# Kernel optimization log

Hardware: AMD Instinct MI355X
Metric: run time of the kernel (lower is better)

Reference implementation:

```python
import jax, jax.numpy as jnp
import numpy as np


def _fake_quant(x, clip_val, level):
    """PACT-style non-negative fake quantization with STE on rounding.

    clamp to [0, clip_val], quantize to `level` uniform levels, dequantize.
    """
    c = clip_val.reshape(())
    scale = c / (level - 1)
    xc = jnp.clip(x, 0.0, c)
    q = jnp.round(xc / scale) * scale
    # straight-through: forward value is q, gradient flows through xc
    return xc + jax.lax.stop_gradient(q - xc)


def setup_inputs() -> dict:
    key = jax.random.key(0)
    k1, k2 = jax.random.split(key)
    B, M, K, N = 8, 4096, 64, 4096
    x1 = jax.random.uniform(k1, (B, M, K), dtype=jnp.float32)
    x2 = jax.random.uniform(k2, (B, K, N), dtype=jnp.float32)
    clip_val1 = jnp.ones((1,), dtype=jnp.float32)
    clip_val2 = jnp.ones((1,), dtype=jnp.float32)
    return {"x1": x1, "x2": x2, "clip_val1": clip_val1,
            "clip_val2": clip_val2, "level": 256}


def reference(x1, x2, clip_val1, clip_val2, level):
    q1 = _fake_quant(x1, clip_val1, level)  # [B, M, K]
    q2 = _fake_quant(x2, clip_val2, level)  # [B, K, N]
    return jnp.matmul(q1, q2)               # [B, M, N]
```

## Files before the change

### kernel.cpp

```cpp
#include <hip/hip_runtime.h>
#include <hip/hip_bf16.h>


#define BATCH 8
#define MDIM 4096
#define KDIM 64
#define NDIM 4096

typedef __attribute__((ext_vector_type(4))) unsigned short u16x4;
typedef __attribute__((ext_vector_type(8))) short s16x8;
typedef __attribute__((ext_vector_type(4))) float f32x4;

__device__ __forceinline__ unsigned short qcode(float x, float c, float inv) {
    float xc = fminf(fmaxf(x, 0.0f), c);
    float k = rintf(xc * inv);
    return (unsigned short)(__float_as_uint(k) >> 16);
}

#define QA_BLOCKS 2048

__global__ void quant_both(const float* __restrict__ x1, const float* __restrict__ x2,
                           unsigned short* __restrict__ qA, unsigned short* __restrict__ qBt,
                           const float* __restrict__ c1p, const float* __restrict__ c2p,
                           const int* __restrict__ lvp) {
    __shared__ unsigned short T[64 * 68];
    const int t = threadIdx.x;
    const float lvm1 = (float)(lvp[0] - 1);

    if (blockIdx.x < QA_BLOCKS) {
        const float c = c1p[0], inv = lvm1 / c;
        int i = blockIdx.x * 256 + t;
        float4 v = ((const float4*)x1)[i];
        u16x4 o;
        o[0] = qcode(v.x, c, inv);
        o[1] = qcode(v.y, c, inv);
        o[2] = qcode(v.z, c, inv);
        o[3] = qcode(v.w, c, inv);
        ((u16x4*)qA)[i] = o;
        return;
    }

    const float c = c2p[0], inv = lvm1 / c;
    int bi = blockIdx.x - QA_BLOCKS;
    int b = bi >> 6;
    int n0 = (bi & 63) * 64;

    const float* src = x2 + (size_t)b * KDIM * NDIM + n0;
#pragma unroll
    for (int it = 0; it < 4; ++it) {
        int qi = t + it * 256;
        int k = qi >> 4, c4 = qi & 15;
        float4 v = *(const float4*)(src + (size_t)k * NDIM + c4 * 4);
        u16x4 o;
        o[0] = qcode(v.x, c, inv);
        o[1] = qcode(v.y, c, inv);
        o[2] = qcode(v.z, c, inv);
        o[3] = qcode(v.w, c, inv);
        *(u16x4*)&T[k * 68 + c4 * 4] = o;
    }
    __syncthreads();

    unsigned short* dst = qBt + ((size_t)b * NDIM + n0) * KDIM;
#pragma unroll
    for (int it = 0; it < 4; ++it) {
        int qi = t + it * 256;
        int n = qi >> 4, c4 = qi & 15;
        u16x4 o;
        o[0] = T[(c4 * 4 + 0) * 68 + n];
        o[1] = T[(c4 * 4 + 1) * 68 + n];
        o[2] = T[(c4 * 4 + 2) * 68 + n];
        o[3] = T[(c4 * 4 + 3) * 68 + n];
        *(u16x4*)(dst + (size_t)n * KDIM + c4 * 4) = o;
    }
}

__global__ __launch_bounds__(256)
void gemm_q(const unsigned short* __restrict__ qA, const unsigned short* __restrict__ qBt,
            const float* __restrict__ c1p, const float* __restrict__ c2p,
            const int* __restrict__ lvp, float* __restrict__ out) {
    const int b = blockIdx.z, mt = blockIdx.y, nt = blockIdx.x;
    const int t = threadIdx.x;
    const int lane = t & 63, w = t >> 6;
    const int wr = (w >> 1) * 64, wc = (w & 1) * 64;
    const int r16 = lane & 15, kq = lane >> 4;

    const unsigned short* pA =
        qA + ((size_t)b * MDIM + mt * 128 + wr + r16) * KDIM + kq * 8;
    const unsigned short* pB =
        qBt + ((size_t)b * NDIM + nt * 128 + wc + r16) * KDIM + kq * 8;

    f32x4 acc[4][4] = {};
#pragma unroll
    for (int ks = 0; ks < 2; ++ks) {
        s16x8 a[4], bf[4];
#pragma unroll
        for (int mf = 0; mf < 4; ++mf)
            a[mf] = *(const s16x8*)(pA + mf * 16 * KDIM + ks * 32);
#pragma unroll
        for (int nf = 0; nf < 4; ++nf)
            bf[nf] = *(const s16x8*)(pB + nf * 16 * KDIM + ks * 32);
#pragma unroll
        for (int mf = 0; mf < 4; ++mf)
#pragma unroll
            for (int nf = 0; nf < 4; ++nf)
                acc[mf][nf] = __builtin_amdgcn_mfma_f32_16x16x32_bf16(
                    bf[nf], a[mf], acc[mf][nf], 0, 0, 0);
    }

    const float c1 = c1p[0], c2 = c2p[0];
    const float lvm1 = (float)(lvp[0] - 1);
    const float s = (c1 / lvm1) * (c2 / lvm1);

    size_t obase = (size_t)b * MDIM * NDIM;
    const int m0 = mt * 128 + wr, n0 = nt * 128 + wc;
#pragma unroll
    for (int mf = 0; mf < 4; ++mf) {
        int m = m0 + mf * 16 + r16;
        float* orow = out + obase + (size_t)m * NDIM;
#pragma unroll
        for (int nf = 0; nf < 4; ++nf) {
            int nb = n0 + nf * 16 + kq * 4;
            float4 v;
            v.x = acc[mf][nf][0] * s;
            v.y = acc[mf][nf][1] * s;
            v.z = acc[mf][nf][2] * s;
            v.w = acc[mf][nf][3] * s;
            *(float4*)(orow + nb) = v;
        }
    }
}

extern "C" void kernel_launch(void* const* d_in, const int* in_sizes, int n_in,
                              void* d_out, int out_size, void* d_ws, size_t ws_size,
                              hipStream_t stream) {
    const float* x1 = (const float*)d_in[0];
    const float* x2 = (const float*)d_in[1];
    const float* c1 = (const float*)d_in[2];
    const float* c2 = (const float*)d_in[3];
    const int* lv   = (const int*)d_in[4];
    float* out = (float*)d_out;

    unsigned short* qA = (unsigned short*)d_ws;
    unsigned short* qB = qA + (size_t)BATCH * MDIM * KDIM;

    quant_both<<<QA_BLOCKS + BATCH * (NDIM / 64), 256, 0, stream>>>(
        x1, x2, qA, qB, c1, c2, lv);
    gemm_q<<<dim3(NDIM / 128, MDIM / 128, BATCH), 256, 0, stream>>>(
        qA, qB, c1, c2, lv, out);
}
```

Before: 133.4 us.

## Stage GEMM operand tiles in swizzled LDS and use nontemporal output stores

The GEMM kernel now loads the 128x64 A and B tiles cooperatively into shared memory with an XOR swizzle, then reads MFMA fragments from LDS instead of each wave fetching its fragments straight from global memory. This cuts redundant global and L2 traffic, since several waves share rows, and gives coalesced 16-byte loads. Output stores also switch to nontemporal to avoid polluting the cache with the large fp32 result. The cost is 32 KB of LDS per block and a barrier, which may lower occupancy. The kernel is likely bound by output writes, so the gain may be limited.

```diff
diff --git a/kernel.cpp b/kernel.cpp
--- a/kernel.cpp
+++ b/kernel.cpp
@@ -78,27 +78,48 @@
 void gemm_q(const unsigned short* __restrict__ qA, const unsigned short* __restrict__ qBt,
             const float* __restrict__ c1p, const float* __restrict__ c2p,
             const int* __restrict__ lvp, float* __restrict__ out) {
+    __shared__ unsigned short As[128 * 64];
+    __shared__ unsigned short Bs[128 * 64];
+
     const int b = blockIdx.z, mt = blockIdx.y, nt = blockIdx.x;
     const int t = threadIdx.x;
+
+    const unsigned short* gA = qA + ((size_t)b * MDIM + mt * 128) * KDIM;
+    const unsigned short* gB = qBt + ((size_t)b * NDIM + nt * 128) * KDIM;
+
+#pragma unroll
+    for (int it = 0; it < 4; ++it) {
+        int qi = t + it * 256;
+        int row = qi >> 3, c8 = qi & 7;
+        s16x8 va = *(const s16x8*)(gA + (size_t)row * KDIM + c8 * 8);
+        s16x8 vb = *(const s16x8*)(gB + (size_t)row * KDIM + c8 * 8);
+        int off = (row * 128 + c8 * 16) ^ ((row & 7) << 4);
+        *(s16x8*)((char*)As + off) = va;
+        *(s16x8*)((char*)Bs + off) = vb;
+    }
+    __syncthreads();
+
     const int lane = t & 63, w = t >> 6;
     const int wr = (w >> 1) * 64, wc = (w & 1) * 64;
     const int r16 = lane & 15, kq = lane >> 4;
 
-    const unsigned short* pA =
-        qA + ((size_t)b * MDIM + mt * 128 + wr + r16) * KDIM + kq * 8;
-    const unsigned short* pB =
-        qBt + ((size_t)b * NDIM + nt * 128 + wc + r16) * KDIM + kq * 8;
-
     f32x4 acc[4][4] = {};
 #pragma unroll
     for (int ks = 0; ks < 2; ++ks) {
+        const int kb = ks * 64 + kq * 16;
         s16x8 a[4], bf[4];
 #pragma unroll
-        for (int mf = 0; mf < 4; ++mf)
-            a[mf] = *(const s16x8*)(pA + mf * 16 * KDIM + ks * 32);
+        for (int mf = 0; mf < 4; ++mf) {
+            int row = wr + mf * 16 + r16;
+            int off = (row * 128 + kb) ^ ((row & 7) << 4);
+            a[mf] = *(const s16x8*)((const char*)As + off);
+        }
 #pragma unroll
-        for (int nf = 0; nf < 4; ++nf)
-            bf[nf] = *(const s16x8*)(pB + nf * 16 * KDIM + ks * 32);
+        for (int nf = 0; nf < 4; ++nf) {
+            int row = wc + nf * 16 + r16;
+            int off = (row * 128 + kb) ^ ((row & 7) << 4);
+            bf[nf] = *(const s16x8*)((const char*)Bs + off);
+        }
 #pragma unroll
         for (int mf = 0; mf < 4; ++mf)
 #pragma unroll
@@ -119,13 +140,12 @@
         float* orow = out + obase + (size_t)m * NDIM;
 #pragma unroll
         for (int nf = 0; nf < 4; ++nf) {
-            int nb = n0 + nf * 16 + kq * 4;
-            float4 v;
-            v.x = acc[mf][nf][0] * s;
-            v.y = acc[mf][nf][1] * s;
-            v.z = acc[mf][nf][2] * s;
-            v.w = acc[mf][nf][3] * s;
-            *(float4*)(orow + nb) = v;
+            f32x4 v;
+            v[0] = acc[mf][nf][0] * s;
+            v[1] = acc[mf][nf][1] * s;
+            v[2] = acc[mf][nf][2] * s;
+            v[3] = acc[mf][nf][3] * s;
+            __builtin_nontemporal_store(v, (f32x4*)(orow + n0 + nf * 16 + kq * 4));
         }
     }
 }
```

Measured after the change: 163.5 us. 22.6% more time.

## Restructure GEMM to row-strip blocks with LDS-staged B and coalesced output stores

Applied to the files above, without the earlier changes.

Each block now owns a 32-row strip of the output for one batch and loops over all 32 column tiles of 128, staging each B tile into swizzled LDS and keeping its A fragments in registers for the whole strip. Accumulators are scaled and written into an LDS buffer, then stored as full contiguous rows, so output writes are fully coalesced. The starting column tile is rotated per block to spread L2 traffic. The cost is fewer, longer-lived blocks (1024 of them), two barriers per tile, and extra LDS round trips for both B and the results.

```diff
diff --git a/kernel.cpp b/kernel.cpp
--- a/kernel.cpp
+++ b/kernel.cpp
@@ -78,56 +78,117 @@
 void gemm_q(const unsigned short* __restrict__ qA, const unsigned short* __restrict__ qBt,
             const float* __restrict__ c1p, const float* __restrict__ c2p,
             const int* __restrict__ lvp, float* __restrict__ out) {
-    const int b = blockIdx.z, mt = blockIdx.y, nt = blockIdx.x;
+    __shared__ __align__(16) unsigned char smem[36864];
+    unsigned short* As = (unsigned short*)smem;
+    unsigned short* Bs = (unsigned short*)(smem + 4096);
+    float* R = (float*)(smem + 20480);
+
+    const int mt = blockIdx.x, b = blockIdx.y;
     const int t = threadIdx.x;
     const int lane = t & 63, w = t >> 6;
-    const int wr = (w >> 1) * 64, wc = (w & 1) * 64;
     const int r16 = lane & 15, kq = lane >> 4;
-
-    const unsigned short* pA =
-        qA + ((size_t)b * MDIM + mt * 128 + wr + r16) * KDIM + kq * 8;
-    const unsigned short* pB =
-        qBt + ((size_t)b * NDIM + nt * 128 + wc + r16) * KDIM + kq * 8;
-
-    f32x4 acc[4][4] = {};
-#pragma unroll
-    for (int ks = 0; ks < 2; ++ks) {
-        s16x8 a[4], bf[4];
-#pragma unroll
-        for (int mf = 0; mf < 4; ++mf)
-            a[mf] = *(const s16x8*)(pA + mf * 16 * KDIM + ks * 32);
-#pragma unroll
-        for (int nf = 0; nf < 4; ++nf)
-            bf[nf] = *(const s16x8*)(pB + nf * 16 * KDIM + ks * 32);
-#pragma unroll
-        for (int mf = 0; mf < 4; ++mf)
-#pragma unroll
-            for (int nf = 0; nf < 4; ++nf)
-                acc[mf][nf] = __builtin_amdgcn_mfma_f32_16x16x32_bf16(
-                    bf[nf], a[mf], acc[mf][nf], 0, 0, 0);
-    }
 
     const float c1 = c1p[0], c2 = c2p[0];
     const float lvm1 = (float)(lvp[0] - 1);
     const float s = (c1 / lvm1) * (c2 / lvm1);
-
-    size_t obase = (size_t)b * MDIM * NDIM;
-    const int m0 = mt * 128 + wr, n0 = nt * 128 + wc;
-#pragma unroll
-    for (int mf = 0; mf < 4; ++mf) {
-        int m = m0 + mf * 16 + r16;
-        float* orow = out + obase + (size_t)m * NDIM;
-#pragma unroll
-        for (int nf = 0; nf < 4; ++nf) {
-            int nb = n0 + nf * 16 + kq * 4;
-            float4 v;
-            v.x = acc[mf][nf][0] * s;
-            v.y = acc[mf][nf][1] * s;
-            v.z = acc[mf][nf][2] * s;
-            v.w = acc[mf][nf][3] * s;
-            *(float4*)(orow + nb) = v;
+    const size_t obase = (size_t)b * MDIM * NDIM;
+    const unsigned short* gBbase = qBt + (size_t)b * NDIM * KDIM;
+
+    {
+        int row = t >> 3, c8 = t & 7;
+        s16x8 va = *(const s16x8*)(qA + ((size_t)b * MDIM + mt * 32 + row) * KDIM + c8 * 8);
+        int off = (row * 128 + c8 * 16) ^ ((row & 7) << 4);
+        *(s16x8*)((char*)As + off) = va;
+    }
+    const int i0 = mt & 31;
+#define STAGE_B(ic)                                                            \
+    {                                                                          \
+        const unsigned short* gB = gBbase + (size_t)(ic) * 128 * KDIM;         \
+        _Pragma("unroll")                                                      \
+        for (int it = 0; it < 4; ++it) {                                       \
+            int qi = t + it * 256;                                             \
+            int row = qi >> 3, c8 = qi & 7;                                    \
+            s16x8 vb = *(const s16x8*)(gB + (size_t)row * KDIM + c8 * 8);      \
+            int off = (row * 128 + c8 * 16) ^ ((row & 7) << 4);                \
+            *(s16x8*)((char*)Bs + off) = vb;                                   \
+        }                                                                      \
+    }
+    STAGE_B(i0);
+    __syncthreads();
+
+    s16x8 afrag[2][2];
+#pragma unroll
+    for (int mf = 0; mf < 2; ++mf)
+#pragma unroll
+        for (int ks = 0; ks < 2; ++ks) {
+            int row = mf * 16 + r16;
+            int off = (row * 128 + ks * 64 + kq * 16) ^ ((row & 7) << 4);
+            afrag[mf][ks] = *(const s16x8*)((const char*)As + off);
         }
-    }
+
+#define MFMA_REPACK()                                                          \
+    {                                                                          \
+        f32x4 acc[2][2] = {};                                                  \
+        _Pragma("unroll")                                                      \
+        for (int ks = 0; ks < 2; ++ks) {                                       \
+            const int kb = ks * 64 + kq * 16;                                  \
+            s16x8 bf[2];                                                       \
+            _Pragma("unroll")                                                  \
+            for (int nf = 0; nf < 2; ++nf) {                                   \
+                int row = w * 32 + nf * 16 + r16;                              \
+                int off = (row * 128 + kb) ^ ((row & 7) << 4);                 \
+                bf[nf] = *(const s16x8*)((const char*)Bs + off);               \
+            }                                                                  \
+            _Pragma("unroll")                                                  \
+            for (int mf = 0; mf < 2; ++mf)                                     \
+                _Pragma("unroll")                                              \
+                for (int nf = 0; nf < 2; ++nf)                                 \
+                    acc[mf][nf] = __builtin_amdgcn_mfma_f32_16x16x32_bf16(     \
+                        afrag[mf][ks], bf[nf], acc[mf][nf], 0, 0, 0);          \
+        }                                                                      \
+        _Pragma("unroll")                                                      \
+        for (int mf = 0; mf < 2; ++mf)                                         \
+            _Pragma("unroll")                                                  \
+            for (int nf = 0; nf < 2; ++nf) {                                   \
+                int col = w * 32 + nf * 16 + r16;                              \
+                _Pragma("unroll")                                              \
+                for (int ii = 0; ii < 4; ++ii) {                               \
+                    int lr = mf * 16 + kq * 4 + ii;                            \
+                    int byte = (lr * 512 + col * 4) ^ ((lr & 7) << 4);         \
+                    *(float*)((char*)R + byte) = acc[mf][nf][ii] * s;          \
+                }                                                              \
+            }                                                                  \
+    }
+
+#define STORE_R(ic)                                                            \
+    {                                                                          \
+        _Pragma("unroll")                                                      \
+        for (int k2 = 0; k2 < 4; ++k2) {                                       \
+            int lr = w * 8 + k2 * 2 + (lane >> 5);                             \
+            int byte = (lr * 512 + (lane & 31) * 16) ^ ((lr & 7) << 4);        \
+            f32x4 v = *(const f32x4*)((const char*)R + byte);                  \
+            float* dst = out + obase + (size_t)(mt * 32 + lr) * NDIM           \
+                       + (ic) * 128 + (lane & 31) * 4;                         \
+            *(f32x4*)dst = v;                                                  \
+        }                                                                      \
+    }
+
+    MFMA_REPACK();
+    __syncthreads();
+
+    for (int j = 1; j < 32; ++j) {
+        const int ic = (mt + j) & 31;
+        const int ip = (mt + j - 1) & 31;
+        STORE_R(ip);
+        STAGE_B(ic);
+        __syncthreads();
+        MFMA_REPACK();
+        __syncthreads();
+    }
+    STORE_R((mt + 31) & 31);
+#undef STAGE_B
+#undef MFMA_REPACK
+#undef STORE_R
 }
 
 extern "C" void kernel_launch(void* const* d_in, const int* in_sizes, int n_in,
@@ -145,6 +206,6 @@
 
     quant_both<<<QA_BLOCKS + BATCH * (NDIM / 64), 256, 0, stream>>>(
         x1, x2, qA, qB, c1, c2, lv);
-    gemm_q<<<dim3(NDIM / 128, MDIM / 128, BATCH), 256, 0, stream>>>(
+    gemm_q<<<dim3(MDIM / 32, BATCH), 256, 0, stream>>>(
         qA, qB, c1, c2, lv, out);
 }
```

After: 131.2 us. About the same (-1.6%).
